# Kernel optimization log

Measured on AMD Instinct MI355X. Metric: run time of the kernel, lower is better.

Reference implementation:

```python
import jax, jax.numpy as jnp
import numpy as np

NUM_HEADS = 16
HEAD_DIM = 64


def setup_inputs() -> dict:
    key = jax.random.key(0)
    ks = jax.random.split(key, 9)
    B, S, E = 16, 577, 1024
    return {
        "hidden_states": jax.random.normal(ks[0], (B, S, E), dtype=jnp.float32),
        "q_w": jax.random.normal(ks[1], (E, E), dtype=jnp.float32) * 0.02,
        "q_b": jax.random.normal(ks[2], (E,), dtype=jnp.float32) * 0.02,
        "v_w": jax.random.normal(ks[3], (E, E), dtype=jnp.float32) * 0.02,
        "v_b": jax.random.normal(ks[4], (E,), dtype=jnp.float32) * 0.02,
        "out_w": jax.random.normal(ks[5], (E, E), dtype=jnp.float32) * 0.02,
        "out_b": jax.random.normal(ks[6], (E,), dtype=jnp.float32) * 0.02,
        "share_key": jax.random.normal(ks[7], (1, NUM_HEADS, HEAD_DIM, 1), dtype=jnp.float32) * 0.1,
        "share_bias": jax.random.normal(ks[8], (NUM_HEADS, S, S), dtype=jnp.float32) * 0.05,
        "layer": 10,
    }


def reference(hidden_states, q_w, q_b, v_w, v_b, out_w, out_b, share_key, share_bias, layer):
    # layer >= START_SHARE_LAYER (9): ShareKey.cal_attention branch.
    B, S, E = hidden_states.shape
    H, D = NUM_HEADS, HEAD_DIM
    scale = D ** -0.5

    # projections (torch Linear: x @ W.T + b)
    q = (hidden_states @ q_w.T + q_b) * scale          # [B,S,E]
    v = hidden_states @ v_w.T + v_b                    # [B,S,E]
    q = q.reshape(B, S, H, D).transpose(0, 2, 1, 3)    # [B,H,S,D]
    v = v.reshape(B, S, H, D).transpose(0, 2, 1, 3)    # [B,H,S,D]

    # rank-1 learned-key scores: matmul(q, key[1,H,D,1]) -> [B,H,S,1]
    scores = jnp.einsum("bhsd,hd->bhs", q, share_key[0, :, :, 0])  # [B,H,S]
    # expand along last axis to [B,H,S,S] and add per-layer learned bias
    attn = scores[..., None] + share_bias[None]         # [B,H,S,S]
    attn = jax.nn.softmax(attn, axis=-1)

    # attn @ V, merge heads, output projection
    out = jnp.einsum("bhij,bhjd->bhid", attn, v)        # [B,H,S,D]
    out = out.transpose(0, 2, 1, 3).reshape(B, S, E)
    out = out @ out_w.T + out_b
    return out
```

## Files before the change

### kernel.cpp

```cpp
#include <hip/hip_runtime.h>


typedef __attribute__((ext_vector_type(4))) float f32x4;
typedef __attribute__((ext_vector_type(4))) unsigned int u32x4;

__device__ __forceinline__ unsigned short f2h(float f) {
  union { _Float16 h; unsigned short u; } x;
  x.h = (_Float16)f;
  return x.u;
}

__device__ __forceinline__ void mfma16(f32x4& d, u32x4 a, u32x4 b) {
  asm("v_mfma_f32_16x16x32_f16 %0, %1, %2, %0" : "+v"(d) : "v"(a), "v"(b));
}

__global__ __launch_bounds__(256) void prep_hs_kernel(const float* __restrict__ X,
                                                      unsigned short* __restrict__ Y) {
  int idx = blockIdx.x * 256 + threadIdx.x;
  int n = idx << 2;
  int row = n >> 10;
  int col = n & 1023;
  int b = row / 584;
  int s = row - b * 584;
  unsigned short o0 = 0, o1 = 0, o2 = 0, o3 = 0;
  if (s < 577) {
    const float4 v = *(const float4*)(X + (((size_t)(b * 577 + s)) << 10) + col);
    o0 = f2h(v.x); o1 = f2h(v.y); o2 = f2h(v.z); o3 = f2h(v.w);
  }
  ushort4 o; o.x = o0; o.y = o1; o.z = o2; o.w = o3;
  *(ushort4*)(Y + n) = o;
}

__global__ __launch_bounds__(256) void prep_w_kernel(const float* __restrict__ X,
                                                     unsigned short* __restrict__ Y) {
  int idx = blockIdx.x * 256 + threadIdx.x;
  int n = idx << 2;
  const float4 v = *(const float4*)(X + n);
  ushort4 o; o.x = f2h(v.x); o.y = f2h(v.y); o.z = f2h(v.z); o.w = f2h(v.w);
  *(ushort4*)(Y + n) = o;
}

__global__ __launch_bounds__(256) void softmax_kernel(const float* __restrict__ SB,
                                                      unsigned short* __restrict__ P) {
  const int i = blockIdx.x;
  const int h = blockIdx.y;
  unsigned short* prow = P + ((size_t)h * 640 + i) * 608;
  const int tid = threadIdx.x;
  if (i >= 577) {
    for (int j = tid; j < 608; j += 256) prow[j] = 0;
    return;
  }
  const float* row = SB + ((size_t)h * 577 + i) * 577;
  __shared__ float buf[577];
  __shared__ float redm[4];
  __shared__ float reds[4];
  float lmax = -3.0e38f;
  for (int j = tid; j < 577; j += 256) { float v = row[j]; buf[j] = v; lmax = fmaxf(lmax, v); }
  #pragma unroll
  for (int off = 32; off > 0; off >>= 1) lmax = fmaxf(lmax, __shfl_xor(lmax, off));
  if ((tid & 63) == 0) redm[tid >> 6] = lmax;
  __syncthreads();
  const float m = fmaxf(fmaxf(redm[0], redm[1]), fmaxf(redm[2], redm[3]));
  float lsum = 0.f;
  for (int j = tid; j < 577; j += 256) { float e = __expf(buf[j] - m); buf[j] = e; lsum += e; }
  #pragma unroll
  for (int off = 32; off > 0; off >>= 1) lsum += __shfl_xor(lsum, off);
  if ((tid & 63) == 0) reds[tid >> 6] = lsum;
  __syncthreads();
  const float inv = 1.f / (reds[0] + reds[1] + reds[2] + reds[3]);
  for (int j = tid; j < 608; j += 256)
    prow[j] = (j < 577) ? f2h(buf[j] * inv) : (unsigned short)0;
}

template<int BIASROW, int OUTF32, int CHECKM>
__global__ __launch_bounds__(256) void gemm128_kernel(
    const unsigned short* __restrict__ A, int lda,
    const unsigned short* __restrict__ B, int ldb,
    const float* __restrict__ bias,
    void* __restrict__ Cv, int ldc, int Mstore, int K)
{
  __shared__ unsigned short As[128 * 40];
  __shared__ unsigned short Bs[128 * 40];
  const int tid  = threadIdx.x;
  const int lane = tid & 63;
  const int w    = tid >> 6;
  const int wm = w >> 1, wn = w & 1;
  const int m0 = blockIdx.x * 128, n0 = blockIdx.y * 128;
  const int srow = tid >> 2;
  const int scol = (tid & 3) << 3;
  const int l15 = lane & 15;
  const int lhi = lane >> 4;

  const unsigned short* Ap0 = A + (size_t)(m0 + srow) * lda + scol;
  const unsigned short* Ap1 = Ap0 + (size_t)64 * lda;
  const unsigned short* Bp0 = B + (size_t)(n0 + srow) * ldb + scol;
  const unsigned short* Bp1 = Bp0 + (size_t)64 * ldb;

  f32x4 acc[4][4] = {};

  for (int k0 = 0; k0 < K; k0 += 32) {
    u32x4 a0 = *(const u32x4*)(Ap0 + k0);
    u32x4 a1 = *(const u32x4*)(Ap1 + k0);
    u32x4 b0 = *(const u32x4*)(Bp0 + k0);
    u32x4 b1 = *(const u32x4*)(Bp1 + k0);
    __syncthreads();
    *(u32x4*)&As[srow * 40 + scol]        = a0;
    *(u32x4*)&As[(64 + srow) * 40 + scol] = a1;
    *(u32x4*)&Bs[srow * 40 + scol]        = b0;
    *(u32x4*)&Bs[(64 + srow) * 40 + scol] = b1;
    __syncthreads();
    u32x4 af[4], bv[4];
    #pragma unroll
    for (int i = 0; i < 4; i++)
      af[i] = *(const u32x4*)&As[(wm * 64 + i * 16 + l15) * 40 + (lhi << 3)];
    #pragma unroll
    for (int i = 0; i < 4; i++)
      bv[i] = *(const u32x4*)&Bs[(wn * 64 + i * 16 + l15) * 40 + (lhi << 3)];
    #pragma unroll
    for (int i = 0; i < 4; i++)
      #pragma unroll
      for (int j = 0; j < 4; j++)
        mfma16(acc[i][j], af[i], bv[j]);
  }

  const int rb = m0 + wm * 64 + (lhi << 2);
  const int cb = n0 + wn * 64 + l15;
  #pragma unroll
  for (int i = 0; i < 4; i++) {
    #pragma unroll
    for (int r = 0; r < 4; r++) {
      const int row = rb + i * 16 + r;
      if (CHECKM && row >= Mstore) continue;
      const float rbias = BIASROW ? bias[row] : 0.f;
      #pragma unroll
      for (int j = 0; j < 4; j++) {
        const int col = cb + j * 16;
        const float v = acc[i][j][r] + (BIASROW ? rbias : bias[col]);
        if (OUTF32) ((float*)Cv)[(size_t)row * ldc + col] = v;
        else        ((unsigned short*)Cv)[(size_t)row * ldc + col] = f2h(v);
      }
    }
  }
}

__global__ __launch_bounds__(256) void gemm_pv_kernel(
    const unsigned short* __restrict__ P,
    const unsigned short* __restrict__ VT,
    unsigned short* __restrict__ Oh)
{
  __shared__ unsigned short As[64 * 40];
  __shared__ unsigned short Bs[64 * 40];
  const int tid  = threadIdx.x;
  const int lane = tid & 63;
  const int w    = tid >> 6;
  const int wm = w >> 1, wn = w & 1;
  const int mt = blockIdx.x;
  const int g  = blockIdx.y;
  const int b = g >> 4, h = g & 15;
  const int l15 = lane & 15, lhi = lane >> 4;
  const int srow = tid >> 2, scol = (tid & 3) << 3;

  const unsigned short* Ap = P  + ((size_t)h * 640 + mt * 64 + srow) * 608 + scol;
  const unsigned short* Bp = VT + ((size_t)(h * 64 + srow)) * 9344 + b * 584 + scol;

  f32x4 acc[2][2] = {};

  for (int k0 = 0; k0 < 608; k0 += 32) {
    u32x4 a  = *(const u32x4*)(Ap + k0);
    u32x4 bv = *(const u32x4*)(Bp + k0);
    __syncthreads();
    *(u32x4*)&As[srow * 40 + scol] = a;
    *(u32x4*)&Bs[srow * 40 + scol] = bv;
    __syncthreads();
    u32x4 af[2], bf2[2];
    #pragma unroll
    for (int i = 0; i < 2; i++) {
      af[i]  = *(const u32x4*)&As[(wm * 32 + i * 16 + l15) * 40 + (lhi << 3)];
      bf2[i] = *(const u32x4*)&Bs[(wn * 32 + i * 16 + l15) * 40 + (lhi << 3)];
    }
    #pragma unroll
    for (int i = 0; i < 2; i++)
      #pragma unroll
      for (int j = 0; j < 2; j++)
        mfma16(acc[i][j], af[i], bf2[j]);
  }

  const int ib = mt * 64 + wm * 32 + (lhi << 2);
  const int cb = wn * 32 + l15;
  #pragma unroll
  for (int i = 0; i < 2; i++) {
    #pragma unroll
    for (int r = 0; r < 4; r++) {
      const int ii = ib + i * 16 + r;
      if (ii < 577) {
        unsigned short* op = Oh + (((size_t)b * 577 + ii) << 10) + h * 64 + cb;
        #pragma unroll
        for (int j = 0; j < 2; j++) op[j * 16] = f2h(acc[i][j][r]);
      }
    }
  }
}

extern "C" void kernel_launch(void* const* d_in, const int* in_sizes, int n_in,
                              void* d_out, int out_size, void* d_ws, size_t ws_size,
                              hipStream_t stream) {
  (void)in_sizes; (void)n_in; (void)out_size; (void)ws_size;
  const float* hs    = (const float*)d_in[0];
  const float* v_w   = (const float*)d_in[3];
  const float* v_b   = (const float*)d_in[4];
  const float* out_w = (const float*)d_in[5];
  const float* out_b = (const float*)d_in[6];
  const float* sb    = (const float*)d_in[8];
  float* out = (float*)d_out;

  char* ws = (char*)d_ws;
  constexpr size_t HS_SZ = (size_t)9344 * 1024 * 2;
  constexpr size_t W_SZ  = (size_t)1024 * 1024 * 2;
  constexpr size_t VT_SZ = (size_t)1024 * 9344 * 2 + 256;
  unsigned short* hs_bf = (unsigned short*)(ws);
  unsigned short* vw_bf = (unsigned short*)(ws + HS_SZ);
  unsigned short* ow_bf = (unsigned short*)(ws + HS_SZ + W_SZ);
  unsigned short* vt    = (unsigned short*)(ws + HS_SZ + 2 * W_SZ);
  unsigned short* pmat  = (unsigned short*)(ws + HS_SZ + 2 * W_SZ + VT_SZ);

  prep_hs_kernel<<<9344, 256, 0, stream>>>(hs, hs_bf);
  prep_w_kernel<<<1024, 256, 0, stream>>>(v_w, vw_bf);
  prep_w_kernel<<<1024, 256, 0, stream>>>(out_w, ow_bf);
  softmax_kernel<<<dim3(640, 16), 256, 0, stream>>>(sb, pmat);
  gemm128_kernel<1, 0, 0><<<dim3(8, 73), 256, 0, stream>>>(vw_bf, 1024, hs_bf, 1024, v_b,
                                                           (void*)vt, 9344, 0, 1024);
  gemm_pv_kernel<<<dim3(10, 256), 256, 0, stream>>>(pmat, vt, hs_bf);
  gemm128_kernel<0, 1, 1><<<dim3(73, 8), 256, 0, stream>>>(hs_bf, 1024, ow_bf, 1024, out_b,
                                                           (void*)out, 1024, 9232, 1024);
}
```

Measured before the change: 265.6 us.

## Use direct global-to-LDS loads in GEMMs and batch PV GEMM across batches per head

Replaces register-staged global loads plus LDS stores with global_load_lds direct transfers in a unified GEMM kernel, removing the LDS padding and adding a trailing barrier. The PV GEMM is rewritten to use the same 128x128 tile kernel, with each head's probability matrix multiplied against all 16 batches' V at once (N = 16*64). This reuses P tiles across batches and gives larger MFMA tiles. In exchange, the loads are no longer overlapped with the previous tile's compute, and the unpadded LDS layout may cause bank conflicts.

```diff
diff --git a/kernel.cpp b/kernel.cpp
--- a/kernel.cpp
+++ b/kernel.cpp
@@ -12,6 +12,12 @@
 
 __device__ __forceinline__ void mfma16(f32x4& d, u32x4 a, u32x4 b) {
   asm("v_mfma_f32_16x16x32_f16 %0, %1, %2, %0" : "+v"(d) : "v"(a), "v"(b));
+}
+
+__device__ __forceinline__ void gl_lds16(const unsigned short* g, unsigned short* l) {
+  __builtin_amdgcn_global_load_lds(
+      (const __attribute__((address_space(1))) unsigned int*)g,
+      (__attribute__((address_space(3))) unsigned int*)l, 16, 0, 0);
 }
 
 __global__ __launch_bounds__(256) void prep_hs_kernel(const float* __restrict__ X,
@@ -72,55 +78,70 @@
     prow[j] = (j < 577) ? f2h(buf[j] * inv) : (unsigned short)0;
 }
 
-template<int BIASROW, int OUTF32, int CHECKM>
-__global__ __launch_bounds__(256) void gemm128_kernel(
+template<int MODE>
+__global__ __launch_bounds__(256) void gemm_glds_kernel(
     const unsigned short* __restrict__ A, int lda,
     const unsigned short* __restrict__ B, int ldb,
     const float* __restrict__ bias,
-    void* __restrict__ Cv, int ldc, int Mstore, int K)
+    void* __restrict__ Cv, int ldc, int K)
 {
-  __shared__ unsigned short As[128 * 40];
-  __shared__ unsigned short Bs[128 * 40];
+  __shared__ unsigned short As[128 * 32];
+  __shared__ unsigned short Bs[128 * 32];
   const int tid  = threadIdx.x;
   const int lane = tid & 63;
   const int w    = tid >> 6;
   const int wm = w >> 1, wn = w & 1;
   const int m0 = blockIdx.x * 128, n0 = blockIdx.y * 128;
-  const int srow = tid >> 2;
-  const int scol = (tid & 3) << 3;
+  const int hh = (MODE == 1) ? blockIdx.z : 0;
   const int l15 = lane & 15;
   const int lhi = lane >> 4;
 
-  const unsigned short* Ap0 = A + (size_t)(m0 + srow) * lda + scol;
-  const unsigned short* Ap1 = Ap0 + (size_t)64 * lda;
-  const unsigned short* Bp0 = B + (size_t)(n0 + srow) * ldb + scol;
-  const unsigned short* Bp1 = Bp0 + (size_t)64 * ldb;
+  const int lr = lane >> 2;
+  const int lc = (lane & 3) << 3;
+
+  if (MODE == 1) A += (size_t)hh * 640 * 608;
+
+  const unsigned short* gA0 = A + (size_t)(m0 + w * 32 + lr) * lda + lc;
+  const unsigned short* gA1 = gA0 + (size_t)16 * lda;
+
+  const unsigned short* gB0;
+  const unsigned short* gB1;
+  if (MODE == 1) {
+    const int nb0 = n0 + w * 32 + lr;
+    const int nb1 = nb0 + 16;
+    gB0 = B + (size_t)(hh * 64 + (nb0 & 63)) * 9344 + (nb0 >> 6) * 584 + lc;
+    gB1 = B + (size_t)(hh * 64 + (nb1 & 63)) * 9344 + (nb1 >> 6) * 584 + lc;
+  } else {
+    gB0 = B + (size_t)(n0 + w * 32 + lr) * ldb + lc;
+    gB1 = gB0 + (size_t)16 * ldb;
+  }
+
+  unsigned short* lA0 = As + (w * 32) * 32;
+  unsigned short* lA1 = As + (w * 32 + 16) * 32;
+  unsigned short* lB0 = Bs + (w * 32) * 32;
+  unsigned short* lB1 = Bs + (w * 32 + 16) * 32;
 
   f32x4 acc[4][4] = {};
 
   for (int k0 = 0; k0 < K; k0 += 32) {
-    u32x4 a0 = *(const u32x4*)(Ap0 + k0);
-    u32x4 a1 = *(const u32x4*)(Ap1 + k0);
-    u32x4 b0 = *(const u32x4*)(Bp0 + k0);
-    u32x4 b1 = *(const u32x4*)(Bp1 + k0);
-    __syncthreads();
-    *(u32x4*)&As[srow * 40 + scol]        = a0;
-    *(u32x4*)&As[(64 + srow) * 40 + scol] = a1;
-    *(u32x4*)&Bs[srow * 40 + scol]        = b0;
-    *(u32x4*)&Bs[(64 + srow) * 40 + scol] = b1;
+    gl_lds16(gA0 + k0, lA0);
+    gl_lds16(gA1 + k0, lA1);
+    gl_lds16(gB0 + k0, lB0);
+    gl_lds16(gB1 + k0, lB1);
     __syncthreads();
     u32x4 af[4], bv[4];
     #pragma unroll
     for (int i = 0; i < 4; i++)
-      af[i] = *(const u32x4*)&As[(wm * 64 + i * 16 + l15) * 40 + (lhi << 3)];
+      af[i] = *(const u32x4*)&As[(wm * 64 + i * 16 + l15) * 32 + (lhi << 3)];
     #pragma unroll
     for (int i = 0; i < 4; i++)
-      bv[i] = *(const u32x4*)&Bs[(wn * 64 + i * 16 + l15) * 40 + (lhi << 3)];
+      bv[i] = *(const u32x4*)&Bs[(wn * 64 + i * 16 + l15) * 32 + (lhi << 3)];
     #pragma unroll
     for (int i = 0; i < 4; i++)
       #pragma unroll
       for (int j = 0; j < 4; j++)
         mfma16(acc[i][j], af[i], bv[j]);
+    __syncthreads();
   }
 
   const int rb = m0 + wm * 64 + (lhi << 2);
@@ -130,72 +151,31 @@
     #pragma unroll
     for (int r = 0; r < 4; r++) {
       const int row = rb + i * 16 + r;
-      if (CHECKM && row >= Mstore) continue;
-      const float rbias = BIASROW ? bias[row] : 0.f;
-      #pragma unroll
-      for (int j = 0; j < 4; j++) {
-        const int col = cb + j * 16;
-        const float v = acc[i][j][r] + (BIASROW ? rbias : bias[col]);
-        if (OUTF32) ((float*)Cv)[(size_t)row * ldc + col] = v;
-        else        ((unsigned short*)Cv)[(size_t)row * ldc + col] = f2h(v);
-      }
-    }
-  }
-}
-
-__global__ __launch_bounds__(256) void gemm_pv_kernel(
-    const unsigned short* __restrict__ P,
-    const unsigned short* __restrict__ VT,
-    unsigned short* __restrict__ Oh)
-{
-  __shared__ unsigned short As[64 * 40];
-  __shared__ unsigned short Bs[64 * 40];
-  const int tid  = threadIdx.x;
-  const int lane = tid & 63;
-  const int w    = tid >> 6;
-  const int wm = w >> 1, wn = w & 1;
-  const int mt = blockIdx.x;
-  const int g  = blockIdx.y;
-  const int b = g >> 4, h = g & 15;
-  const int l15 = lane & 15, lhi = lane >> 4;
-  const int srow = tid >> 2, scol = (tid & 3) << 3;
-
-  const unsigned short* Ap = P  + ((size_t)h * 640 + mt * 64 + srow) * 608 + scol;
-  const unsigned short* Bp = VT + ((size_t)(h * 64 + srow)) * 9344 + b * 584 + scol;
-
-  f32x4 acc[2][2] = {};
-
-  for (int k0 = 0; k0 < 608; k0 += 32) {
-    u32x4 a  = *(const u32x4*)(Ap + k0);
-    u32x4 bv = *(const u32x4*)(Bp + k0);
-    __syncthreads();
-    *(u32x4*)&As[srow * 40 + scol] = a;
-    *(u32x4*)&Bs[srow * 40 + scol] = bv;
-    __syncthreads();
-    u32x4 af[2], bf2[2];
-    #pragma unroll
-    for (int i = 0; i < 2; i++) {
-      af[i]  = *(const u32x4*)&As[(wm * 32 + i * 16 + l15) * 40 + (lhi << 3)];
-      bf2[i] = *(const u32x4*)&Bs[(wn * 32 + i * 16 + l15) * 40 + (lhi << 3)];
-    }
-    #pragma unroll
-    for (int i = 0; i < 2; i++)
-      #pragma unroll
-      for (int j = 0; j < 2; j++)
-        mfma16(acc[i][j], af[i], bf2[j]);
-  }
-
-  const int ib = mt * 64 + wm * 32 + (lhi << 2);
-  const int cb = wn * 32 + l15;
-  #pragma unroll
-  for (int i = 0; i < 2; i++) {
-    #pragma unroll
-    for (int r = 0; r < 4; r++) {
-      const int ii = ib + i * 16 + r;
-      if (ii < 577) {
-        unsigned short* op = Oh + (((size_t)b * 577 + ii) << 10) + h * 64 + cb;
+      if (MODE == 0) {
+        const float rbias = bias[row];
         #pragma unroll
-        for (int j = 0; j < 2; j++) op[j * 16] = f2h(acc[i][j][r]);
+        for (int j = 0; j < 4; j++) {
+          const int col = cb + j * 16;
+          ((unsigned short*)Cv)[(size_t)row * ldc + col] = f2h(acc[i][j][r] + rbias);
+        }
+      } else if (MODE == 1) {
+        if (row < 577) {
+          #pragma unroll
+          for (int j = 0; j < 4; j++) {
+            const int n = cb + j * 16;
+            const int b = n >> 6, d = n & 63;
+            ((unsigned short*)Cv)[(((size_t)b * 577 + row) << 10) + hh * 64 + d] =
+                f2h(acc[i][j][r]);
+          }
+        }
+      } else {
+        if (row < 9232) {
+          #pragma unroll
+          for (int j = 0; j < 4; j++) {
+            const int col = cb + j * 16;
+            ((float*)Cv)[(size_t)row * ldc + col] = acc[i][j][r] + bias[col];
+          }
+        }
       }
     }
   }
@@ -217,19 +197,20 @@
   constexpr size_t HS_SZ = (size_t)9344 * 1024 * 2;
   constexpr size_t W_SZ  = (size_t)1024 * 1024 * 2;
   constexpr size_t VT_SZ = (size_t)1024 * 9344 * 2 + 256;
-  unsigned short* hs_bf = (unsigned short*)(ws);
-  unsigned short* vw_bf = (unsigned short*)(ws + HS_SZ);
-  unsigned short* ow_bf = (unsigned short*)(ws + HS_SZ + W_SZ);
-  unsigned short* vt    = (unsigned short*)(ws + HS_SZ + 2 * W_SZ);
-  unsigned short* pmat  = (unsigned short*)(ws + HS_SZ + 2 * W_SZ + VT_SZ);
-
-  prep_hs_kernel<<<9344, 256, 0, stream>>>(hs, hs_bf);
-  prep_w_kernel<<<1024, 256, 0, stream>>>(v_w, vw_bf);
-  prep_w_kernel<<<1024, 256, 0, stream>>>(out_w, ow_bf);
+  unsigned short* hs_f16 = (unsigned short*)(ws);
+  unsigned short* vw_f16 = (unsigned short*)(ws + HS_SZ);
+  unsigned short* ow_f16 = (unsigned short*)(ws + HS_SZ + W_SZ);
+  unsigned short* vt     = (unsigned short*)(ws + HS_SZ + 2 * W_SZ);
+  unsigned short* pmat   = (unsigned short*)(ws + HS_SZ + 2 * W_SZ + VT_SZ);
+
+  prep_hs_kernel<<<9344, 256, 0, stream>>>(hs, hs_f16);
+  prep_w_kernel<<<1024, 256, 0, stream>>>(v_w, vw_f16);
+  prep_w_kernel<<<1024, 256, 0, stream>>>(out_w, ow_f16);
   softmax_kernel<<<dim3(640, 16), 256, 0, stream>>>(sb, pmat);
-  gemm128_kernel<1, 0, 0><<<dim3(8, 73), 256, 0, stream>>>(vw_bf, 1024, hs_bf, 1024, v_b,
-                                                           (void*)vt, 9344, 0, 1024);
-  gemm_pv_kernel<<<dim3(10, 256), 256, 0, stream>>>(pmat, vt, hs_bf);
-  gemm128_kernel<0, 1, 1><<<dim3(73, 8), 256, 0, stream>>>(hs_bf, 1024, ow_bf, 1024, out_b,
-                                                           (void*)out, 1024, 9232, 1024);
-}
+  gemm_glds_kernel<0><<<dim3(8, 73), 256, 0, stream>>>(vw_f16, 1024, hs_f16, 1024, v_b,
+                                                       (void*)vt, 9344, 1024);
+  gemm_glds_kernel<1><<<dim3(5, 8, 16), 256, 0, stream>>>(pmat, 608, vt, 0, nullptr,
+                                                          (void*)hs_f16, 0, 608);
+  gemm_glds_kernel<2><<<dim3(73, 8), 256, 0, stream>>>(hs_f16, 1024, ow_f16, 1024, out_b,
+                                                       (void*)out, 1024, 1024);
+}
```

Measured after the change: 250.6 us. 5.6% less time.
